# Performance work log

Hardware: AMD Instinct MI355X
Metric: run time of the kernel (lower is better)

Reference implementation:

```python
import jax, jax.numpy as jnp
import numpy as np
import math

B, T, C = 2, 2048, 1024
H = 16
D = C // H  # 64


def setup_inputs() -> dict:
    key = jax.random.key(0)
    ks = jax.random.split(key, 12)
    s = 1.0 / math.sqrt(C)
    inp = {
        "q": jax.random.normal(ks[0], (B, T, C), dtype=jnp.float32),
        "k": jax.random.normal(ks[1], (B, T, C), dtype=jnp.float32),
        "v": jax.random.normal(ks[2], (B, T, C), dtype=jnp.float32),
        # causal mask, broadcastable to [B, H, T, T]; 0 -> masked
        "mask": jnp.tril(jnp.ones((T, T), dtype=jnp.int32))[None, None, :, :],
        "Wq": jax.random.normal(ks[3], (C, C), dtype=jnp.float32) * s,
        "bq": jnp.zeros((C,), dtype=jnp.float32),
        "Wk": jax.random.normal(ks[4], (C, C), dtype=jnp.float32) * s,
        "bk": jnp.zeros((C,), dtype=jnp.float32),
        "Wv": jax.random.normal(ks[5], (C, C), dtype=jnp.float32) * s,
        "bv": jnp.zeros((C,), dtype=jnp.float32),
        "Wo": jax.random.normal(ks[6], (C, C), dtype=jnp.float32) * s,
        "bo": jnp.zeros((C,), dtype=jnp.float32),
    }
    return inp


def reference(q, k, v, mask, Wq, bq, Wk, bk, Wv, bv, Wo, bo):
    # Linear projections (torch Linear: x @ W.T + b), split into heads -> [B,H,T,D]
    qh = (q @ Wq.T + bq).reshape(B, T, H, D).transpose(0, 2, 1, 3)
    kh = (k @ Wk.T + bk).reshape(B, T, H, D).transpose(0, 2, 1, 3)
    vh = (v @ Wv.T + bv).reshape(B, T, H, D).transpose(0, 2, 1, 3)
    # scaled dot-product attention with full [B,H,T,T] scores (faithful to source)
    scores = jnp.einsum("bhqd,bhkd->bhqk", qh, kh) / math.sqrt(D)
    scores = jnp.where(mask == 0, -jnp.inf, scores)
    attn = jax.nn.softmax(scores, axis=-1)  # dropout = identity (eval mode)
    out = jnp.einsum("bhqk,bhkd->bhqd", attn, vh)
    out = out.transpose(0, 2, 1, 3).reshape(B, T, C)
    return out @ Wo.T + bo
```

## Files before the change

kernel.cpp:

```cpp
#include <hip/hip_runtime.h>
#include <hip/hip_bf16.h>
#include <cstdint>
#include <cstddef>

#define B_ 2
#define T_ 2048
#define C_ 1024
#define H_ 16
#define D_ 64

typedef unsigned short u16;
typedef unsigned int u32;

typedef __bf16 bf16x8 __attribute__((ext_vector_type(8)));
typedef float f32x4 __attribute__((ext_vector_type(4)));

#define QSCALE 0.18033688011112042f
#define DEFER_THR 11.5f

union BFQ {
    uint4 q;
    bf16x8 v;
    u16 s[8];
};

__device__ __forceinline__ float bf2f(u16 s) {
    union { u32 u; float f; } x;
    x.u = ((u32)s) << 16;
    return x.f;
}

__device__ __forceinline__ u16 f2bf(float f) {
    union { __bf16 h; u16 u; } c;
    c.h = (__bf16)f;
    return c.u;
}

__device__ __forceinline__ void gl_lds16(const u16* g, u16* l) {
    __builtin_amdgcn_global_load_lds(
        (const __attribute__((address_space(1))) u32*)g,
        (__attribute__((address_space(3))) u32*)l, 16, 0, 0);
}

__global__ void cvt3_kernel(const float* __restrict__ i0, const float* __restrict__ i1,
                            const float* __restrict__ i2, u16* __restrict__ o0,
                            u16* __restrict__ o1, u16* __restrict__ o2, int n4) {
    const float* in = blockIdx.z == 0 ? i0 : (blockIdx.z == 1 ? i1 : i2);
    u16* out = blockIdx.z == 0 ? o0 : (blockIdx.z == 1 ? o1 : o2);
    int i = blockIdx.x * blockDim.x + threadIdx.x;
    int stride = gridDim.x * blockDim.x;
    for (; i < n4; i += stride) {
        float4 f = reinterpret_cast<const float4*>(in)[i];
        ushort4 o;
        o.x = f2bf(f.x);
        o.y = f2bf(f.y);
        o.z = f2bf(f.z);
        o.w = f2bf(f.w);
        reinterpret_cast<ushort4*>(out)[i] = o;
    }
}

__global__ void cvt4_kernel(const float* __restrict__ i0, const float* __restrict__ i1,
                            const float* __restrict__ i2, const float* __restrict__ i3,
                            u16* __restrict__ o0, u16* __restrict__ o1,
                            u16* __restrict__ o2, u16* __restrict__ o3, int n4) {
    int z = blockIdx.z;
    const float* in = z == 0 ? i0 : (z == 1 ? i1 : (z == 2 ? i2 : i3));
    u16* out = z == 0 ? o0 : (z == 1 ? o1 : (z == 2 ? o2 : o3));
    int i = blockIdx.x * blockDim.x + threadIdx.x;
    int stride = gridDim.x * blockDim.x;
    for (; i < n4; i += stride) {
        float4 f = reinterpret_cast<const float4*>(in)[i];
        ushort4 o;
        o.x = f2bf(f.x);
        o.y = f2bf(f.y);
        o.z = f2bf(f.z);
        o.w = f2bf(f.w);
        reinterpret_cast<ushort4*>(out)[i] = o;
    }
}

template <int OUT_BF16>
__device__ __forceinline__ void gemm_body(const u16* __restrict__ A,
                                          const u16* __restrict__ Bw,
                                          const float* __restrict__ bias,
                                          void* __restrict__ Cout,
                                          int M, int N, int K) {
    __shared__ u16 As[2][128 * 64];
    __shared__ u16 Bs[2][64 * 64];

    const int tid = threadIdx.x;
    const int lane = tid & 63;
    const int wave = tid >> 6;
    const int wm = wave >> 1, wn = wave & 1;
    const int g = lane >> 4, r = lane & 15;
    const int m0 = blockIdx.y * 128, n0 = blockIdx.x * 64;

    f32x4 acc[4][2] = {};

    const int lrow = lane >> 3;
    const int lcolS = ((lane & 7) ^ (lane >> 3)) * 8;
    const u16* Abase = A + (size_t)(m0 + lrow) * K + lcolS;
    const u16* Bbase = Bw + (size_t)(n0 + lrow) * K + lcolS;

#pragma unroll
    for (int c = 0; c < 4; ++c) {
        int ca = 4 * wave + c;
        gl_lds16(Abase + (size_t)(8 * ca) * K, As[0] + ca * 512);
    }
#pragma unroll
    for (int c = 0; c < 2; ++c) {
        int cb = 2 * wave + c;
        gl_lds16(Bbase + (size_t)(8 * cb) * K, Bs[0] + cb * 512);
    }
    __syncthreads();

    int cur = 0;
    for (int k0 = 0; k0 < K; k0 += 64) {
        if (k0 + 64 < K) {
#pragma unroll
            for (int c = 0; c < 4; ++c) {
                int ca = 4 * wave + c;
                gl_lds16(Abase + (size_t)(8 * ca) * K + k0 + 64, As[cur ^ 1] + ca * 512);
            }
#pragma unroll
            for (int c = 0; c < 2; ++c) {
                int cb = 2 * wave + c;
                gl_lds16(Bbase + (size_t)(8 * cb) * K + k0 + 64, Bs[cur ^ 1] + cb * 512);
            }
        }

#pragma unroll
        for (int kk = 0; kk < 2; ++kk) {
            bf16x8 af[4], bfv[2];
#pragma unroll
            for (int mt = 0; mt < 4; ++mt) {
                int row = wm * 64 + mt * 16 + r;
                BFQ u;
                u.q = *(const uint4*)(As[cur] + row * 64 + (((kk * 4 + g) ^ (r & 7)) * 8));
                af[mt] = u.v;
            }
#pragma unroll
            for (int nt = 0; nt < 2; ++nt) {
                int row = wn * 32 + nt * 16 + r;
                BFQ u;
                u.q = *(const uint4*)(Bs[cur] + row * 64 + (((kk * 4 + g) ^ (r & 7)) * 8));
                bfv[nt] = u.v;
            }
            __builtin_amdgcn_s_setprio(1);
#pragma unroll
            for (int mt = 0; mt < 4; ++mt)
#pragma unroll
                for (int nt = 0; nt < 2; ++nt)
                    acc[mt][nt] = __builtin_amdgcn_mfma_f32_16x16x32_bf16(af[mt], bfv[nt], acc[mt][nt], 0, 0, 0);
            __builtin_amdgcn_s_setprio(0);
        }
        __syncthreads();
        cur ^= 1;
    }

#pragma unroll
    for (int mt = 0; mt < 4; ++mt) {
#pragma unroll
        for (int nt = 0; nt < 2; ++nt) {
            int n = n0 + wn * 32 + nt * 16 + r;
            float bv = bias[n];
#pragma unroll
            for (int j = 0; j < 4; ++j) {
                int m = m0 + wm * 64 + mt * 16 + g * 4 + j;
                float val = acc[mt][nt][j] + bv;
                if (OUT_BF16)
                    ((u16*)Cout)[(size_t)m * N + n] = f2bf(val);
                else
                    ((float*)Cout)[(size_t)m * N + n] = val;
            }
        }
    }
}

__global__ __launch_bounds__(256, 3) void gemm3_kernel(
    const u16* __restrict__ A0, const u16* __restrict__ A1, const u16* __restrict__ A2,
    const u16* __restrict__ W0, const u16* __restrict__ W1, const u16* __restrict__ W2,
    const float* __restrict__ b0, const float* __restrict__ b1, const float* __restrict__ b2,
    u16* __restrict__ C0, u16* __restrict__ C1, u16* __restrict__ C2,
    int M, int N, int K) {
    int z = blockIdx.z;
    const u16* A = z == 0 ? A0 : (z == 1 ? A1 : A2);
    const u16* W = z == 0 ? W0 : (z == 1 ? W1 : W2);
    const float* bias = z == 0 ? b0 : (z == 1 ? b1 : b2);
    u16* C = z == 0 ? C0 : (z == 1 ? C1 : C2);
    gemm_body<1>(A, W, bias, C, M, N, K);
}

__global__ __launch_bounds__(256, 3) void gemm_f32_kernel(const u16* __restrict__ A,
                                                          const u16* __restrict__ W,
                                                          const float* __restrict__ bias,
                                                          float* __restrict__ C,
                                                          int M, int N, int K) {
    gemm_body<0>(A, W, bias, C, M, N, K);
}


__device__ __forceinline__ void softmax_swapped(f32x4* s, int domask, int kv0, int qcol0,
                                                int g, int r, float& m_run, float& l_run,
                                                f32x4* o_acc, u16* pl) {
    float sv[4][4];
#pragma unroll
    for (int nt = 0; nt < 4; ++nt) {
#pragma unroll
        for (int j = 0; j < 4; ++j) {
            float x = s[nt][j];
            if (domask) {
                int kg = kv0 + nt * 16 + g * 4 + j;
                int qg = qcol0 + r;
                x = (kg <= qg) ? x : -1e30f;
            }
            sv[nt][j] = x;
        }
    }
    float m0 = fmaxf(fmaxf(sv[0][0], sv[0][1]), fmaxf(sv[0][2], sv[0][3]));
    float m1 = fmaxf(fmaxf(sv[1][0], sv[1][1]), fmaxf(sv[1][2], sv[1][3]));
    float m2 = fmaxf(fmaxf(sv[2][0], sv[2][1]), fmaxf(sv[2][2], sv[2][3]));
    float m3 = fmaxf(fmaxf(sv[3][0], sv[3][1]), fmaxf(sv[3][2], sv[3][3]));
    float rm = fmaxf(fmaxf(m0, m1), fmaxf(m2, m3));
    rm = fmaxf(rm, __shfl_xor(rm, 16));
    rm = fmaxf(rm, __shfl_xor(rm, 32));

    if (!__all(rm - m_run <= DEFER_THR)) {
        float mnew = fmaxf(m_run, rm);
        float fac = __builtin_amdgcn_exp2f(m_run - mnew);
        l_run *= fac;
        m_run = mnew;
#pragma unroll
        for (int j = 0; j < 4; ++j) {
            float fo = __shfl(fac, g * 4 + j);
#pragma unroll
            for (int nt = 0; nt < 4; ++nt) o_acc[nt][j] *= fo;
        }
    }

    float p[4][4];
#pragma unroll
    for (int nt = 0; nt < 4; ++nt)
#pragma unroll
        for (int j = 0; j < 4; ++j)
            p[nt][j] = __builtin_amdgcn_exp2f(sv[nt][j] - m_run);

    float s0 = (p[0][0] + p[0][1]) + (p[0][2] + p[0][3]);
    float s1 = (p[1][0] + p[1][1]) + (p[1][2] + p[1][3]);
    float s2 = (p[2][0] + p[2][1]) + (p[2][2] + p[2][3]);
    float s3 = (p[3][0] + p[3][1]) + (p[3][2] + p[3][3]);
    float rs = (s0 + s1) + (s2 + s3);
    rs += __shfl_xor(rs, 16);
    rs += __shfl_xor(rs, 32);
    l_run += rs;

    const int sw = (r & 7) << 3;
#pragma unroll
    for (int nt = 0; nt < 4; ++nt) {
        uint2 w;
        w.x = (u32)f2bf(p[nt][0]) | ((u32)f2bf(p[nt][1]) << 16);
        w.y = (u32)f2bf(p[nt][2]) | ((u32)f2bf(p[nt][3]) << 16);
        *(uint2*)&pl[(r * 64 + nt * 16 + g * 4) ^ sw] = w;
    }
}

__global__ __launch_bounds__(256, 2) void attn_kernel(const u16* __restrict__ Qp,
                                                      const u16* __restrict__ Kp,
                                                      const u16* __restrict__ Vp,
                                                      u16* __restrict__ OP0,
                                                      u16* __restrict__ OP1,
                                                      float* __restrict__ ML) {
    __shared__ u16 Kl[2][64 * 64];
    __shared__ u16 Vt[64 * 64];
    __shared__ u16 Pl[4][2][16 * 64];

    const int tid = threadIdx.x, lane = tid & 63, wave = tid >> 6;
    const int g = lane >> 4, r = lane & 15;

    const int lid = blockIdx.x;
    const int xcd = lid & 7;
    const int idx = lid >> 3;
    const int bh = xcd * 4 + (idx >> 5);
    const int iz = idx & 31;
    const int i = iz & 15;
    const int z = iz >> 4;
    const int b = bh >> 4, h = bh & 15;
    const int qA0 = i * 64;
    const int qB0 = (31 - i) * 64;

    const u16* Qbh = Qp + ((size_t)b * T_) * C_ + h * 64;
    const u16* Kbh = Kp + ((size_t)b * T_) * C_ + h * 64;
    const u16* Vbh = Vp + ((size_t)b * T_) * C_ + h * 64;

    bf16x8 aqA[2], aqB[2];
    {
        const u16* qa = Qbh + (size_t)(qA0 + wave * 16 + r) * C_ + g * 8;
        const u16* qb = Qbh + (size_t)(qB0 + wave * 16 + r) * C_ + g * 8;
        BFQ u0, u1, u2, u3;
        u0.q = *(const uint4*)(qa);
        u1.q = *(const uint4*)(qa + 32);
        u2.q = *(const uint4*)(qb);
        u3.q = *(const uint4*)(qb + 32);
#pragma unroll
        for (int e = 0; e < 8; ++e) {
            u0.s[e] = f2bf(bf2f(u0.s[e]) * QSCALE);
            u1.s[e] = f2bf(bf2f(u1.s[e]) * QSCALE);
            u2.s[e] = f2bf(bf2f(u2.s[e]) * QSCALE);
            u3.s[e] = f2bf(bf2f(u3.s[e]) * QSCALE);
        }
        aqA[0] = u0.v; aqA[1] = u1.v;
        aqB[0] = u2.v; aqB[1] = u3.v;
    }

    float mA = -1e30f, lA = 0.f, mB = -1e30f, lB = 0.f;
    f32x4 oA[4] = {}, oB[4] = {};

    const int klr = lane >> 3;
    const int kgcol = ((lane & 7) ^ klr) * 8;

    const int vp = tid & 31;
    const int vd0 = (tid >> 5) * 8;

#pragma unroll
    for (int c = 0; c < 2; ++c) {
        int rb = wave * 16 + c * 8;
        gl_lds16(Kbh + (size_t)(z * 64 + rb + klr) * C_ + kgcol, Kl[0] + rb * 64);
    }
    BFQ va, vb;
    {
        const u16* vr0 = Vbh + (size_t)(z * 64 + 2 * vp) * C_ + vd0;
        va.q = *(const uint4*)(vr0);
        vb.q = *(const uint4*)(vr0 + C_);
    }
    asm volatile("s_waitcnt vmcnt(0)" ::: "memory");
    __builtin_amdgcn_s_barrier();

    int cur = 0;
    for (int kv0 = z * 64; kv0 <= qB0; kv0 += 128) {
        const int actA = (kv0 <= qA0);
        const int havenext = (kv0 + 128 <= qB0);

        __builtin_amdgcn_s_barrier();

#pragma unroll
        for (int ii = 0; ii < 8; ++ii) {
            int d = vd0 + ii;
            u32 pr = (u32)va.s[ii] | ((u32)vb.s[ii] << 16);
            *(u32*)&Vt[(d * 64 + 2 * vp) ^ ((d & 7) << 3)] = pr;
        }

        if (havenext) {
            const u16* vr0 = Vbh + (size_t)(kv0 + 128 + 2 * vp) * C_ + vd0;
            va.q = *(const uint4*)(vr0);
            vb.q = *(const uint4*)(vr0 + C_);
        }

        BFQ kf[2][4];
#pragma unroll
        for (int kk = 0; kk < 2; ++kk)
#pragma unroll
            for (int nt = 0; nt < 4; ++nt)
                kf[kk][nt].q = *(const uint4*)(Kl[cur] + (nt * 16 + r) * 64 + (((kk * 4 + g) ^ (r & 7)) * 8));

        f32x4 sB[4] = {}, sA[4] = {};
        __builtin_amdgcn_s_setprio(1);
#pragma unroll
        for (int kk = 0; kk < 2; ++kk)
#pragma unroll
            for (int nt = 0; nt < 4; ++nt)
                sB[nt] = __builtin_amdgcn_mfma_f32_16x16x32_bf16(kf[kk][nt].v, aqB[kk], sB[nt], 0, 0, 0);
        if (actA) {
#pragma unroll
            for (int kk = 0; kk < 2; ++kk)
#pragma unroll
                for (int nt = 0; nt < 4; ++nt)
                    sA[nt] = __builtin_amdgcn_mfma_f32_16x16x32_bf16(kf[kk][nt].v, aqA[kk], sA[nt], 0, 0, 0);
        }
        __builtin_amdgcn_s_setprio(0);

        if (havenext) {
#pragma unroll
            for (int c = 0; c < 2; ++c) {
                int rb = wave * 16 + c * 8;
                gl_lds16(Kbh + (size_t)(kv0 + 128 + rb + klr) * C_ + kgcol, Kl[cur ^ 1] + rb * 64);
            }
        }

        softmax_swapped(sB, kv0 == qB0, kv0, qB0 + wave * 16, g, r, mB, lB, oB, Pl[wave][0]);
        if (actA)
            softmax_swapped(sA, kv0 == qA0, kv0, qA0 + wave * 16, g, r, mA, lA, oA, Pl[wave][1]);

        asm volatile("s_waitcnt lgkmcnt(0)" ::: "memory");
        __builtin_amdgcn_s_barrier();

        bf16x8 vf[2][4];
#pragma unroll
        for (int kk = 0; kk < 2; ++kk)
#pragma unroll
            for (int nt = 0; nt < 4; ++nt) {
                int d = nt * 16 + r;
                BFQ u;
                u.q = *(const uint4*)&Vt[(d * 64 + kk * 32 + g * 8) ^ ((d & 7) << 3)];
                vf[kk][nt] = u.v;
            }

        __builtin_amdgcn_s_setprio(1);
#pragma unroll
        for (int kk = 0; kk < 2; ++kk) {
            BFQ ua;
            ua.q = *(const uint4*)&Pl[wave][0][(r * 64 + kk * 32 + g * 8) ^ ((r & 7) << 3)];
#pragma unroll
            for (int nt = 0; nt < 4; ++nt)
                oB[nt] = __builtin_amdgcn_mfma_f32_16x16x32_bf16(ua.v, vf[kk][nt], oB[nt], 0, 0, 0);
        }
        if (actA) {
#pragma unroll
            for (int kk = 0; kk < 2; ++kk) {
                BFQ ua;
                ua.q = *(const uint4*)&Pl[wave][1][(r * 64 + kk * 32 + g * 8) ^ ((r & 7) << 3)];
#pragma unroll
                for (int nt = 0; nt < 4; ++nt)
                    oA[nt] = __builtin_amdgcn_mfma_f32_16x16x32_bf16(ua.v, vf[kk][nt], oA[nt], 0, 0, 0);
            }
        }
        __builtin_amdgcn_s_setprio(0);

        asm volatile("s_waitcnt vmcnt(0)" ::: "memory");
        cur ^= 1;
    }

    u16* OPz = z ? OP1 : OP0;
    u16* Obh = OPz + ((size_t)b * T_) * C_ + h * 64;
    float* MLz = ML + (((size_t)z * 32 + bh) * T_) * 2;
#pragma unroll
    for (int nt = 0; nt < 4; ++nt) {
#pragma unroll
        for (int j = 0; j < 4; ++j) {
            int qgB = qB0 + wave * 16 + g * 4 + j;
            Obh[(size_t)qgB * C_ + nt * 16 + r] = f2bf(oB[nt][j]);
            int qgA = qA0 + wave * 16 + g * 4 + j;
            Obh[(size_t)qgA * C_ + nt * 16 + r] = f2bf(oA[nt][j]);
        }
    }
    if (g == 0) {
        int qgB = qB0 + wave * 16 + r;
        MLz[qgB * 2 + 0] = mB;
        MLz[qgB * 2 + 1] = lB;
        int qgA = qA0 + wave * 16 + r;
        MLz[qgA * 2 + 0] = mA;
        MLz[qgA * 2 + 1] = lA;
    }
}

__global__ void merge_kernel(const u16* __restrict__ O0, const u16* __restrict__ O1,
                             const float* __restrict__ ML, u16* __restrict__ Out) {
    int idx = blockIdx.x * blockDim.x + threadIdx.x;
    size_t base = (size_t)idx * 8;
    int h = (int)((base >> 6) & 15);
    int q = (int)((base >> 10) & (T_ - 1));
    int b = (int)(base >> 21);
    int bh = b * 16 + h;
    const float* ml0 = ML + (((size_t)0 * 32 + bh) * T_ + q) * 2;
    const float* ml1 = ML + (((size_t)1 * 32 + bh) * T_ + q) * 2;
    float m0 = ml0[0], l0 = ml0[1];
    float m1 = ml1[0], l1 = ml1[1];
    float mM = fmaxf(m0, m1);
    float w0 = __builtin_amdgcn_exp2f(m0 - mM);
    float w1 = __builtin_amdgcn_exp2f(m1 - mM);
    float inv = 1.0f / (l0 * w0 + l1 * w1);
    BFQ a, c, o;
    a.q = *(const uint4*)(O0 + base);
    c.q = *(const uint4*)(O1 + base);
#pragma unroll
    for (int e = 0; e < 8; ++e)
        o.s[e] = f2bf((bf2f(a.s[e]) * w0 + bf2f(c.s[e]) * w1) * inv);
    *(uint4*)(Out + base) = o.q;
}

extern "C" void kernel_launch(void* const* d_in, const int* in_sizes, int n_in,
                              void* d_out, int out_size, void* d_ws, size_t ws_size,
                              hipStream_t stream) {
    const float* q = (const float*)d_in[0];
    const float* k = (const float*)d_in[1];
    const float* v = (const float*)d_in[2];
    const float* Wq = (const float*)d_in[4];
    const float* bq = (const float*)d_in[5];
    const float* Wk = (const float*)d_in[6];
    const float* bk = (const float*)d_in[7];
    const float* Wv = (const float*)d_in[8];
    const float* bv = (const float*)d_in[9];
    const float* Wo = (const float*)d_in[10];
    const float* bo = (const float*)d_in[11];

    const size_t NTC = (size_t)B_ * T_ * C_;
    const size_t NW = (size_t)C_ * C_;

    char* ws = (char*)d_ws;
    size_t off = 0;
    u16* qb = (u16*)(ws + off);  off += NTC * 2;
    u16* kb = (u16*)(ws + off);  off += NTC * 2;
    u16* vb = (u16*)(ws + off);  off += NTC * 2;
    u16* Wqb = (u16*)(ws + off); off += NW * 2;
    u16* Wkb = (u16*)(ws + off); off += NW * 2;
    u16* Wvb = (u16*)(ws + off); off += NW * 2;
    u16* Wob = (u16*)(ws + off); off += NW * 2;
    u16* Qp = (u16*)(ws + off);  off += NTC * 2;
    u16* Kp = (u16*)(ws + off);  off += NTC * 2;
    u16* Vp = (u16*)(ws + off);  off += NTC * 2;
    u16* AOb = (u16*)(ws + off); off += NTC * 2;

    u16* OP0 = qb;
    u16* OP1 = kb;
    float* ML = (float*)vb;

    cvt3_kernel<<<dim3(512, 1, 3), 256, 0, stream>>>(q, k, v, qb, kb, vb, (int)(NTC / 4));
    cvt4_kernel<<<dim3(128, 1, 4), 256, 0, stream>>>(Wq, Wk, Wv, Wo, Wqb, Wkb, Wvb, Wob, (int)(NW / 4));

    const int M = B_ * T_;
    dim3 g3(C_ / 64, M / 128, 3);
    gemm3_kernel<<<g3, 256, 0, stream>>>(qb, kb, vb, Wqb, Wkb, Wvb, bq, bk, bv,
                                         Qp, Kp, Vp, M, C_, C_);

    attn_kernel<<<1024, 256, 0, stream>>>(Qp, Kp, Vp, OP0, OP1, ML);

    merge_kernel<<<(int)(NTC / 8 / 256), 256, 0, stream>>>(OP0, OP1, ML, AOb);

    dim3 g1(C_ / 64, M / 128, 1);
    gemm_f32_kernel<<<g1, 256, 0, stream>>>(AOb, Wob, bo, (float*)d_out, M, C_, C_);
}
```

Baseline: 136.1 us.

## Fuse split-KV merge into output GEMM A-loading and merge conversion kernels

The separate merge kernel that combined the two split-KV partial outputs is removed. The output projection GEMM now loads both partials and the softmax stats while staging its A tile, combines them in registers and writes the bf16 result to LDS. This avoids writing and re-reading the merged attention output, at the cost of extra loads and exp work inside the GEMM, which is repeated for each of the 16 N-tile blocks. The input and weight conversion kernels are also merged into one seven-slice launch to save a launch.

```diff
diff --git a/kernel.cpp b/kernel.cpp
--- a/kernel.cpp
+++ b/kernel.cpp
@@ -42,31 +42,26 @@
         (__attribute__((address_space(3))) u32*)l, 16, 0, 0);
 }
 
-__global__ void cvt3_kernel(const float* __restrict__ i0, const float* __restrict__ i1,
-                            const float* __restrict__ i2, u16* __restrict__ o0,
-                            u16* __restrict__ o1, u16* __restrict__ o2, int n4) {
-    const float* in = blockIdx.z == 0 ? i0 : (blockIdx.z == 1 ? i1 : i2);
-    u16* out = blockIdx.z == 0 ? o0 : (blockIdx.z == 1 ? o1 : o2);
-    int i = blockIdx.x * blockDim.x + threadIdx.x;
-    int stride = gridDim.x * blockDim.x;
-    for (; i < n4; i += stride) {
-        float4 f = reinterpret_cast<const float4*>(in)[i];
-        ushort4 o;
-        o.x = f2bf(f.x);
-        o.y = f2bf(f.y);
-        o.z = f2bf(f.z);
-        o.w = f2bf(f.w);
-        reinterpret_cast<ushort4*>(out)[i] = o;
-    }
-}
-
-__global__ void cvt4_kernel(const float* __restrict__ i0, const float* __restrict__ i1,
-                            const float* __restrict__ i2, const float* __restrict__ i3,
-                            u16* __restrict__ o0, u16* __restrict__ o1,
-                            u16* __restrict__ o2, u16* __restrict__ o3, int n4) {
+__global__ void cvt7_kernel(const float* __restrict__ q, const float* __restrict__ k,
+                            const float* __restrict__ v, const float* __restrict__ Wq,
+                            const float* __restrict__ Wk, const float* __restrict__ Wv,
+                            const float* __restrict__ Wo,
+                            u16* __restrict__ qb, u16* __restrict__ kb, u16* __restrict__ vb,
+                            u16* __restrict__ Wqb, u16* __restrict__ Wkb, u16* __restrict__ Wvb,
+                            u16* __restrict__ Wob, int nBig4, int nW4) {
     int z = blockIdx.z;
-    const float* in = z == 0 ? i0 : (z == 1 ? i1 : (z == 2 ? i2 : i3));
-    u16* out = z == 0 ? o0 : (z == 1 ? o1 : (z == 2 ? o2 : o3));
+    const float* in;
+    u16* out;
+    int n4;
+    switch (z) {
+        case 0: in = q;  out = qb;  n4 = nBig4; break;
+        case 1: in = k;  out = kb;  n4 = nBig4; break;
+        case 2: in = v;  out = vb;  n4 = nBig4; break;
+        case 3: in = Wq; out = Wqb; n4 = nW4; break;
+        case 4: in = Wk; out = Wkb; n4 = nW4; break;
+        case 5: in = Wv; out = Wvb; n4 = nW4; break;
+        default: in = Wo; out = Wob; n4 = nW4; break;
+    }
     int i = blockIdx.x * blockDim.x + threadIdx.x;
     int stride = gridDim.x * blockDim.x;
     for (; i < n4; i += stride) {
@@ -192,14 +187,115 @@
     gemm_body<1>(A, W, bias, C, M, N, K);
 }
 
-__global__ __launch_bounds__(256, 3) void gemm_f32_kernel(const u16* __restrict__ A,
-                                                          const u16* __restrict__ W,
-                                                          const float* __restrict__ bias,
-                                                          float* __restrict__ C,
-                                                          int M, int N, int K) {
-    gemm_body<0>(A, W, bias, C, M, N, K);
-}
-
+__global__ __launch_bounds__(256, 3) void gemm_out_kernel(
+    const u16* __restrict__ OP0, const u16* __restrict__ OP1,
+    const float* __restrict__ ML, const u16* __restrict__ Bw,
+    const float* __restrict__ bias, float* __restrict__ Cout,
+    int M, int N, int K) {
+    __shared__ u16 As[2][128 * 64];
+    __shared__ u16 Bs[2][64 * 64];
+
+    const int tid = threadIdx.x;
+    const int lane = tid & 63;
+    const int wave = tid >> 6;
+    const int wm = wave >> 1, wn = wave & 1;
+    const int g = lane >> 4, r = lane & 15;
+    const int m0 = blockIdx.y * 128, n0 = blockIdx.x * 64;
+
+    f32x4 acc[4][2] = {};
+
+    const int lrow = lane >> 3;
+    const int lcolS = ((lane & 7) ^ (lane >> 3)) * 8;
+    const u16* Bbase = Bw + (size_t)(n0 + lrow) * K + lcolS;
+
+    auto stageA = [&](int ca, int k0, int buf) {
+        int row = m0 + 8 * ca + lrow;
+        int col = k0 + lcolS;
+        int b = row >> 11, t = row & (T_ - 1);
+        int bh = b * 16 + (col >> 6);
+        const float* ml0 = ML + (((size_t)bh) * T_ + t) * 2;
+        const float* ml1 = ML + (((size_t)(32 + bh)) * T_ + t) * 2;
+        float m0v = ml0[0], l0 = ml0[1];
+        float m1v = ml1[0], l1 = ml1[1];
+        float mM = fmaxf(m0v, m1v);
+        float w0 = __builtin_amdgcn_exp2f(m0v - mM);
+        float w1 = __builtin_amdgcn_exp2f(m1v - mM);
+        float inv = 1.0f / (l0 * w0 + l1 * w1);
+        w0 *= inv;
+        w1 *= inv;
+        BFQ a0, a1, o;
+        a0.q = *(const uint4*)(OP0 + (size_t)row * K + col);
+        a1.q = *(const uint4*)(OP1 + (size_t)row * K + col);
+#pragma unroll
+        for (int e = 0; e < 8; ++e)
+            o.s[e] = f2bf(bf2f(a0.s[e]) * w0 + bf2f(a1.s[e]) * w1);
+        *(uint4*)(As[buf] + ca * 512 + lane * 8) = o.q;
+    };
+
+#pragma unroll
+    for (int c = 0; c < 4; ++c) stageA(4 * wave + c, 0, 0);
+#pragma unroll
+    for (int c = 0; c < 2; ++c) {
+        int cb = 2 * wave + c;
+        gl_lds16(Bbase + (size_t)(8 * cb) * K, Bs[0] + cb * 512);
+    }
+    __syncthreads();
+
+    int cur = 0;
+    for (int k0 = 0; k0 < K; k0 += 64) {
+        if (k0 + 64 < K) {
+#pragma unroll
+            for (int c = 0; c < 4; ++c) stageA(4 * wave + c, k0 + 64, cur ^ 1);
+#pragma unroll
+            for (int c = 0; c < 2; ++c) {
+                int cb = 2 * wave + c;
+                gl_lds16(Bbase + (size_t)(8 * cb) * K + k0 + 64, Bs[cur ^ 1] + cb * 512);
+            }
+        }
+
+#pragma unroll
+        for (int kk = 0; kk < 2; ++kk) {
+            bf16x8 af[4], bfv[2];
+#pragma unroll
+            for (int mt = 0; mt < 4; ++mt) {
+                int row = wm * 64 + mt * 16 + r;
+                BFQ u;
+                u.q = *(const uint4*)(As[cur] + row * 64 + (((kk * 4 + g) ^ (r & 7)) * 8));
+                af[mt] = u.v;
+            }
+#pragma unroll
+            for (int nt = 0; nt < 2; ++nt) {
+                int row = wn * 32 + nt * 16 + r;
+                BFQ u;
+                u.q = *(const uint4*)(Bs[cur] + row * 64 + (((kk * 4 + g) ^ (r & 7)) * 8));
+                bfv[nt] = u.v;
+            }
+            __builtin_amdgcn_s_setprio(1);
+#pragma unroll
+            for (int mt = 0; mt < 4; ++mt)
+#pragma unroll
+                for (int nt = 0; nt < 2; ++nt)
+                    acc[mt][nt] = __builtin_amdgcn_mfma_f32_16x16x32_bf16(af[mt], bfv[nt], acc[mt][nt], 0, 0, 0);
+            __builtin_amdgcn_s_setprio(0);
+        }
+        __syncthreads();
+        cur ^= 1;
+    }
+
+#pragma unroll
+    for (int mt = 0; mt < 4; ++mt) {
+#pragma unroll
+        for (int nt = 0; nt < 2; ++nt) {
+            int n = n0 + wn * 32 + nt * 16 + r;
+            float bv = bias[n];
+#pragma unroll
+            for (int j = 0; j < 4; ++j) {
+                int m = m0 + wm * 64 + mt * 16 + g * 4 + j;
+                Cout[(size_t)m * N + n] = acc[mt][nt][j] + bv;
+            }
+        }
+    }
+}
 
 __device__ __forceinline__ void softmax_swapped(f32x4* s, int domask, int kv0, int qcol0,
                                                 int g, int r, float& m_run, float& l_run,
@@ -451,31 +547,6 @@
         MLz[qgA * 2 + 0] = mA;
         MLz[qgA * 2 + 1] = lA;
     }
-}
-
-__global__ void merge_kernel(const u16* __restrict__ O0, const u16* __restrict__ O1,
-                             const float* __restrict__ ML, u16* __restrict__ Out) {
-    int idx = blockIdx.x * blockDim.x + threadIdx.x;
-    size_t base = (size_t)idx * 8;
-    int h = (int)((base >> 6) & 15);
-    int q = (int)((base >> 10) & (T_ - 1));
-    int b = (int)(base >> 21);
-    int bh = b * 16 + h;
-    const float* ml0 = ML + (((size_t)0 * 32 + bh) * T_ + q) * 2;
-    const float* ml1 = ML + (((size_t)1 * 32 + bh) * T_ + q) * 2;
-    float m0 = ml0[0], l0 = ml0[1];
-    float m1 = ml1[0], l1 = ml1[1];
-    float mM = fmaxf(m0, m1);
-    float w0 = __builtin_amdgcn_exp2f(m0 - mM);
-    float w1 = __builtin_amdgcn_exp2f(m1 - mM);
-    float inv = 1.0f / (l0 * w0 + l1 * w1);
-    BFQ a, c, o;
-    a.q = *(const uint4*)(O0 + base);
-    c.q = *(const uint4*)(O1 + base);
-#pragma unroll
-    for (int e = 0; e < 8; ++e)
-        o.s[e] = f2bf((bf2f(a.s[e]) * w0 + bf2f(c.s[e]) * w1) * inv);
-    *(uint4*)(Out + base) = o.q;
 }
 
 extern "C" void kernel_launch(void* const* d_in, const int* in_sizes, int n_in,
@@ -508,14 +579,14 @@
     u16* Qp = (u16*)(ws + off);  off += NTC * 2;
     u16* Kp = (u16*)(ws + off);  off += NTC * 2;
     u16* Vp = (u16*)(ws + off);  off += NTC * 2;
-    u16* AOb = (u16*)(ws + off); off += NTC * 2;
 
     u16* OP0 = qb;
     u16* OP1 = kb;
     float* ML = (float*)vb;
 
-    cvt3_kernel<<<dim3(512, 1, 3), 256, 0, stream>>>(q, k, v, qb, kb, vb, (int)(NTC / 4));
-    cvt4_kernel<<<dim3(128, 1, 4), 256, 0, stream>>>(Wq, Wk, Wv, Wo, Wqb, Wkb, Wvb, Wob, (int)(NW / 4));
+    cvt7_kernel<<<dim3(512, 1, 7), 256, 0, stream>>>(q, k, v, Wq, Wk, Wv, Wo,
+                                                     qb, kb, vb, Wqb, Wkb, Wvb, Wob,
+                                                     (int)(NTC / 4), (int)(NW / 4));
 
     const int M = B_ * T_;
     dim3 g3(C_ / 64, M / 128, 3);
@@ -524,8 +595,6 @@
 
     attn_kernel<<<1024, 256, 0, stream>>>(Qp, Kp, Vp, OP0, OP1, ML);
 
-    merge_kernel<<<(int)(NTC / 8 / 256), 256, 0, stream>>>(OP0, OP1, ML, AOb);
-
     dim3 g1(C_ / 64, M / 128, 1);
-    gemm_f32_kernel<<<g1, 256, 0, stream>>>(AOb, Wob, bo, (float*)d_out, M, C_, C_);
-}
+    gemm_out_kernel<<<g1, 256, 0, stream>>>(OP0, OP1, ML, Wob, bo, (float*)d_out, M, C_, C_);
+}
```

Result: slower. 144.8 us (+6.4%).

## Merge conversion kernels and pair adjacent query tiles, heaviest first

Applied to the files above, without the earlier changes.

The two fp32-to-bf16 conversion launches become a single 7-slice launch covering q, k, v and all four weight matrices. In the attention kernel, each block previously took a mirrored pair of query tiles (i, 31-i) so every block had the same causal work. It now takes adjacent tiles (2i, 2i+1), with the index reversed so the longest-running blocks are dispatched first. Adjacent tiles need nearly the same causal K/V range, so shared K/V loads may be reused better. The cost is that per-block work is no longer uniform, so load balance now depends on the heavy-first ordering.

```diff
diff --git a/kernel.cpp b/kernel.cpp
--- a/kernel.cpp
+++ b/kernel.cpp
@@ -42,31 +42,26 @@
         (__attribute__((address_space(3))) u32*)l, 16, 0, 0);
 }
 
-__global__ void cvt3_kernel(const float* __restrict__ i0, const float* __restrict__ i1,
-                            const float* __restrict__ i2, u16* __restrict__ o0,
-                            u16* __restrict__ o1, u16* __restrict__ o2, int n4) {
-    const float* in = blockIdx.z == 0 ? i0 : (blockIdx.z == 1 ? i1 : i2);
-    u16* out = blockIdx.z == 0 ? o0 : (blockIdx.z == 1 ? o1 : o2);
-    int i = blockIdx.x * blockDim.x + threadIdx.x;
-    int stride = gridDim.x * blockDim.x;
-    for (; i < n4; i += stride) {
-        float4 f = reinterpret_cast<const float4*>(in)[i];
-        ushort4 o;
-        o.x = f2bf(f.x);
-        o.y = f2bf(f.y);
-        o.z = f2bf(f.z);
-        o.w = f2bf(f.w);
-        reinterpret_cast<ushort4*>(out)[i] = o;
-    }
-}
-
-__global__ void cvt4_kernel(const float* __restrict__ i0, const float* __restrict__ i1,
-                            const float* __restrict__ i2, const float* __restrict__ i3,
-                            u16* __restrict__ o0, u16* __restrict__ o1,
-                            u16* __restrict__ o2, u16* __restrict__ o3, int n4) {
+__global__ void cvt7_kernel(const float* __restrict__ q, const float* __restrict__ k,
+                            const float* __restrict__ v, const float* __restrict__ Wq,
+                            const float* __restrict__ Wk, const float* __restrict__ Wv,
+                            const float* __restrict__ Wo,
+                            u16* __restrict__ qb, u16* __restrict__ kb, u16* __restrict__ vb,
+                            u16* __restrict__ Wqb, u16* __restrict__ Wkb, u16* __restrict__ Wvb,
+                            u16* __restrict__ Wob, int nBig4, int nW4) {
     int z = blockIdx.z;
-    const float* in = z == 0 ? i0 : (z == 1 ? i1 : (z == 2 ? i2 : i3));
-    u16* out = z == 0 ? o0 : (z == 1 ? o1 : (z == 2 ? o2 : o3));
+    const float* in;
+    u16* out;
+    int n4;
+    switch (z) {
+        case 0: in = q;  out = qb;  n4 = nBig4; break;
+        case 1: in = k;  out = kb;  n4 = nBig4; break;
+        case 2: in = v;  out = vb;  n4 = nBig4; break;
+        case 3: in = Wq; out = Wqb; n4 = nW4; break;
+        case 4: in = Wk; out = Wkb; n4 = nW4; break;
+        case 5: in = Wv; out = Wvb; n4 = nW4; break;
+        default: in = Wo; out = Wob; n4 = nW4; break;
+    }
     int i = blockIdx.x * blockDim.x + threadIdx.x;
     int stride = gridDim.x * blockDim.x;
     for (; i < n4; i += stride) {
@@ -283,11 +278,11 @@
     const int idx = lid >> 3;
     const int bh = xcd * 4 + (idx >> 5);
     const int iz = idx & 31;
-    const int i = iz & 15;
+    const int i = 15 - (iz & 15);
     const int z = iz >> 4;
     const int b = bh >> 4, h = bh & 15;
-    const int qA0 = i * 64;
-    const int qB0 = (31 - i) * 64;
+    const int qA0 = (2 * i) * 64;
+    const int qB0 = (2 * i + 1) * 64;
 
     const u16* Qbh = Qp + ((size_t)b * T_) * C_ + h * 64;
     const u16* Kbh = Kp + ((size_t)b * T_) * C_ + h * 64;
@@ -514,8 +509,9 @@
     u16* OP1 = kb;
     float* ML = (float*)vb;
 
-    cvt3_kernel<<<dim3(512, 1, 3), 256, 0, stream>>>(q, k, v, qb, kb, vb, (int)(NTC / 4));
-    cvt4_kernel<<<dim3(128, 1, 4), 256, 0, stream>>>(Wq, Wk, Wv, Wo, Wqb, Wkb, Wvb, Wob, (int)(NW / 4));
+    cvt7_kernel<<<dim3(512, 1, 7), 256, 0, stream>>>(q, k, v, Wq, Wk, Wv, Wo,
+                                                     qb, kb, vb, Wqb, Wkb, Wvb, Wob,
+                                                     (int)(NTC / 4), (int)(NW / 4));
 
     const int M = B_ * T_;
     dim3 g3(C_ / 64, M / 128, 3);
```

Result: slower. 149.3 us (+9.7%).
